# Kernel tuning notes

Hardware: AMD Instinct MI355X
Metric: run time of the kernel (lower is better)

Reference implementation:

```python
import jax, jax.numpy as jnp
import numpy as np

BATCH = 256
INPUT_DIM = 64
LEVELS = 100
HV_DIM = 10000


def setup_inputs() -> dict:
    key = jax.random.key(0)
    kx, kb = jax.random.split(key)
    x = jax.random.uniform(kx, (BATCH, INPUT_DIM), dtype=jnp.float32)
    base = jax.random.normal(kb, (INPUT_DIM, LEVELS, HV_DIM), dtype=jnp.float32)
    # buffer is L2-normalized along hv_dim at construction time
    base = base / jnp.linalg.norm(base, axis=-1, keepdims=True)
    return {"x": x, "base_hvs": base}


def reference(x, base_hvs):
    D, L, H = base_hvs.shape
    B = x.shape[0]
    xn = jnp.clip(x * (L - 1), 0.0, float(L - 1))          # [B, D]
    lo = jnp.floor(xn).astype(jnp.int32)                    # [B, D]
    hi = jnp.clip(lo + 1, 0, L - 1)                         # [B, D]
    alpha = xn - lo.astype(x.dtype)                         # [B, D]

    def step(acc, inputs):
        bhv, l, h, a = inputs    # bhv: [L, H], l/h/a: [B]
        hv_low = bhv[l]          # [B, H] gather
        hv_high = bhv[h]         # [B, H] gather
        a = a[:, None]
        return acc + (1.0 - a) * hv_low + a * hv_high, None

    init = jnp.zeros((B, H), dtype=x.dtype)
    encoded, _ = jax.lax.scan(step, init, (base_hvs, lo.T, hi.T, alpha.T))
    return encoded / jnp.linalg.norm(encoded, axis=-1, keepdims=True)
```

## Files before the change

### kernel.cpp

```cpp
#include <hip/hip_runtime.h>

#define BATCH   256
#define DIMS    64
#define LEVELS  100
#define HVD     10000

__global__ __launch_bounds__(256) void encode_kernel(
    const float* __restrict__ x,
    const float* __restrict__ base,
    float* __restrict__ out)
{
    __shared__ int   s_off_lo[256];
    __shared__ int   s_off_hi[256];
    __shared__ float s_alpha[256];

    const int tid    = threadIdx.x;
    const int b_tile = blockIdx.x;
    const int h0     = blockIdx.y * 256;

    {
        const int bl = tid >> 6;
        const int d  = tid & 63;
        const int b  = b_tile * 4 + bl;
        float xv = x[b * DIMS + d];
        float xn = xv * (float)(LEVELS - 1);
        xn = fminf(fmaxf(xn, 0.0f), (float)(LEVELS - 1));
        float fl = floorf(xn);
        int   lo = (int)fl;
        int   hi = lo + 1; if (hi > LEVELS - 1) hi = LEVELS - 1;
        s_off_lo[tid] = (d * LEVELS + lo) * HVD;
        s_off_hi[tid] = (d * LEVELS + hi) * HVD;
        s_alpha[tid]  = xn - fl;
    }
    __syncthreads();

    const int bl   = tid >> 6;
    const int lane = tid & 63;
    const int h    = h0 + lane * 4;
    if (h >= HVD) return;
    const int b    = b_tile * 4 + bl;

    const int ebase = bl * 64;
    float4 acc = make_float4(0.f, 0.f, 0.f, 0.f);

    #pragma unroll 8
    for (int d = 0; d < DIMS; ++d) {
        const int   off_lo = s_off_lo[ebase + d];
        const int   off_hi = s_off_hi[ebase + d];
        const float a      = s_alpha[ebase + d];
        const float wl     = 1.0f - a;
        float4 vlo = *(const float4*)(base + off_lo + h);
        float4 vhi = *(const float4*)(base + off_hi + h);
        acc.x += wl * vlo.x + a * vhi.x;
        acc.y += wl * vlo.y + a * vhi.y;
        acc.z += wl * vlo.z + a * vhi.z;
        acc.w += wl * vlo.w + a * vhi.w;
    }

    *(float4*)(out + b * HVD + h) = acc;
}

__global__ __launch_bounds__(256) void normalize_kernel(float* __restrict__ out)
{
    const int b   = blockIdx.x;
    const int tid = threadIdx.x;
    float* row = out + b * HVD;
    const float4* row4 = (const float4*)row;

    float ss = 0.f;
    for (int i = tid; i < HVD / 4; i += 256) {
        float4 v = row4[i];
        ss += v.x * v.x + v.y * v.y + v.z * v.z + v.w * v.w;
    }

    __shared__ float red[256];
    red[tid] = ss;
    __syncthreads();
    #pragma unroll
    for (int s = 128; s > 0; s >>= 1) {
        if (tid < s) red[tid] += red[tid + s];
        __syncthreads();
    }
    const float inv = rsqrtf(red[0]);

    for (int i = tid; i < HVD / 4; i += 256) {
        float4 v = ((float4*)row)[i];
        v.x *= inv; v.y *= inv; v.z *= inv; v.w *= inv;
        ((float4*)row)[i] = v;
    }
}

extern "C" void kernel_launch(void* const* d_in, const int* in_sizes, int n_in,
                              void* d_out, int out_size, void* d_ws, size_t ws_size,
                              hipStream_t stream)
{
    const float* x    = (const float*)d_in[0];
    const float* base = (const float*)d_in[1];
    float*       out  = (float*)d_out;

    dim3 grid(BATCH / 4, (HVD + 255) / 256);
    encode_kernel<<<grid, 256, 0, stream>>>(x, base, out);
    normalize_kernel<<<BATCH, 256, 0, stream>>>(out);
}
```

Measured before the change: 402.7 us.

## Stage base-vector chunks in LDS and split reduction over input dims

The encoder now tiles along the hypervector dimension. Each block loads all 100 levels of one input dim for a 64-wide column slice into shared memory, and all 256 batch rows gather from there, so each base element is read from global memory once rather than once per batch tile. The 64 input dims are split across 8 blocks that write partial sums to workspace. The finish kernel sums those partials, then normalizes. This cuts the redundant global gather traffic on the large base tensor, at the cost of a workspace round trip of 8x the output size and 16 float4 accumulators per thread.

```diff
diff --git a/kernel.cpp b/kernel.cpp
--- a/kernel.cpp
+++ b/kernel.cpp
@@ -4,73 +4,106 @@
 #define DIMS    64
 #define LEVELS  100
 #define HVD     10000
+#define WH      64
+#define NHT     157
+#define DSPLIT  8
+#define DPER    8
+#define LSTRIDE 68
 
 __global__ __launch_bounds__(256) void encode_kernel(
     const float* __restrict__ x,
     const float* __restrict__ base,
-    float* __restrict__ out)
+    float* __restrict__ partial)
 {
-    __shared__ int   s_off_lo[256];
-    __shared__ int   s_off_hi[256];
-    __shared__ float s_alpha[256];
+    __shared__ float s_chunk[LEVELS * LSTRIDE];
+    __shared__ int   s_lohi[DPER][BATCH];
+    __shared__ float s_a[DPER][BATCH];
 
-    const int tid    = threadIdx.x;
-    const int b_tile = blockIdx.x;
-    const int h0     = blockIdx.y * 256;
+    const int tid   = threadIdx.x;
+    const int htile = blockIdx.x;
+    const int split = blockIdx.y;
+    const int h0    = htile * WH;
+    const int d0    = split * DPER;
 
-    {
-        const int bl = tid >> 6;
-        const int d  = tid & 63;
-        const int b  = b_tile * 4 + bl;
-        float xv = x[b * DIMS + d];
-        float xn = xv * (float)(LEVELS - 1);
-        xn = fminf(fmaxf(xn, 0.0f), (float)(LEVELS - 1));
+    for (int k = 0; k < DPER; ++k) {
+        const int dl = k;
+        const int b  = tid;
+        float xv = x[b * DIMS + d0 + dl];
+        float xn = fminf(fmaxf(xv * (float)(LEVELS - 1), 0.0f), (float)(LEVELS - 1));
         float fl = floorf(xn);
         int   lo = (int)fl;
-        int   hi = lo + 1; if (hi > LEVELS - 1) hi = LEVELS - 1;
-        s_off_lo[tid] = (d * LEVELS + lo) * HVD;
-        s_off_hi[tid] = (d * LEVELS + hi) * HVD;
-        s_alpha[tid]  = xn - fl;
-    }
-    __syncthreads();
-
-    const int bl   = tid >> 6;
-    const int lane = tid & 63;
-    const int h    = h0 + lane * 4;
-    if (h >= HVD) return;
-    const int b    = b_tile * 4 + bl;
-
-    const int ebase = bl * 64;
-    float4 acc = make_float4(0.f, 0.f, 0.f, 0.f);
-
-    #pragma unroll 8
-    for (int d = 0; d < DIMS; ++d) {
-        const int   off_lo = s_off_lo[ebase + d];
-        const int   off_hi = s_off_hi[ebase + d];
-        const float a      = s_alpha[ebase + d];
-        const float wl     = 1.0f - a;
-        float4 vlo = *(const float4*)(base + off_lo + h);
-        float4 vhi = *(const float4*)(base + off_hi + h);
-        acc.x += wl * vlo.x + a * vhi.x;
-        acc.y += wl * vlo.y + a * vhi.y;
-        acc.z += wl * vlo.z + a * vhi.z;
-        acc.w += wl * vlo.w + a * vhi.w;
+        int   hi = lo < LEVELS - 1 ? lo + 1 : LEVELS - 1;
+        s_lohi[dl][b] = (lo * LSTRIDE) | ((hi * LSTRIDE) << 16);
+        s_a[dl][b]    = xn - fl;
     }
 
-    *(float4*)(out + b * HVD + h) = acc;
+    const int g  = tid >> 4;
+    const int ci = (tid & 15) * 4;
+    const int wvalid = (HVD - h0) < WH ? (HVD - h0) : WH;
+
+    float4 acc[16];
+    #pragma unroll
+    for (int j = 0; j < 16; ++j) acc[j] = make_float4(0.f, 0.f, 0.f, 0.f);
+
+    for (int dc = 0; dc < DPER; ++dc) {
+        __syncthreads();
+
+        const float* src = base + ((size_t)(d0 + dc) * LEVELS) * (size_t)HVD + h0;
+        for (int i = tid; i < LEVELS * (WH / 4); i += 256) {
+            const int l  = i >> 4;
+            const int cc = (i & 15) * 4;
+            if (cc < wvalid) {
+                float4 v = *(const float4*)(src + (size_t)l * HVD + cc);
+                *(float4*)(&s_chunk[l * LSTRIDE + cc]) = v;
+            }
+        }
+        __syncthreads();
+
+        #pragma unroll
+        for (int j = 0; j < 16; ++j) {
+            const int   b    = g * 16 + j;
+            const int   lohi = s_lohi[dc][b];
+            const float a    = s_a[dc][b];
+            const int   olo  = lohi & 0xffff;
+            const int   ohi  = lohi >> 16;
+            const float wl   = 1.0f - a;
+            float4 vlo = *(const float4*)(&s_chunk[olo + ci]);
+            float4 vhi = *(const float4*)(&s_chunk[ohi + ci]);
+            acc[j].x += wl * vlo.x + a * vhi.x;
+            acc[j].y += wl * vlo.y + a * vhi.y;
+            acc[j].z += wl * vlo.z + a * vhi.z;
+            acc[j].w += wl * vlo.w + a * vhi.w;
+        }
+    }
+
+    if (ci < wvalid) {
+        float* dst = partial + ((size_t)split * BATCH) * (size_t)HVD + h0 + ci;
+        #pragma unroll
+        for (int j = 0; j < 16; ++j) {
+            const int b = g * 16 + j;
+            *(float4*)(dst + (size_t)b * HVD) = acc[j];
+        }
+    }
 }
 
-__global__ __launch_bounds__(256) void normalize_kernel(float* __restrict__ out)
+__global__ __launch_bounds__(256) void finish_kernel(
+    const float* __restrict__ partial,
+    float* __restrict__ out)
 {
     const int b   = blockIdx.x;
     const int tid = threadIdx.x;
-    float* row = out + b * HVD;
-    const float4* row4 = (const float4*)row;
 
     float ss = 0.f;
     for (int i = tid; i < HVD / 4; i += 256) {
-        float4 v = row4[i];
-        ss += v.x * v.x + v.y * v.y + v.z * v.z + v.w * v.w;
+        float4 s = make_float4(0.f, 0.f, 0.f, 0.f);
+        #pragma unroll
+        for (int sp = 0; sp < DSPLIT; ++sp) {
+            const float4 v = *(const float4*)(partial +
+                ((size_t)sp * BATCH + b) * (size_t)HVD + i * 4);
+            s.x += v.x; s.y += v.y; s.z += v.z; s.w += v.w;
+        }
+        *(float4*)(out + (size_t)b * HVD + i * 4) = s;
+        ss += s.x * s.x + s.y * s.y + s.z * s.z + s.w * s.w;
     }
 
     __shared__ float red[256];
@@ -84,9 +117,9 @@
     const float inv = rsqrtf(red[0]);
 
     for (int i = tid; i < HVD / 4; i += 256) {
-        float4 v = ((float4*)row)[i];
+        float4 v = *(float4*)(out + (size_t)b * HVD + i * 4);
         v.x *= inv; v.y *= inv; v.z *= inv; v.w *= inv;
-        ((float4*)row)[i] = v;
+        *(float4*)(out + (size_t)b * HVD + i * 4) = v;
     }
 }
 
@@ -97,8 +130,9 @@
     const float* x    = (const float*)d_in[0];
     const float* base = (const float*)d_in[1];
     float*       out  = (float*)d_out;
+    float*       part = (float*)d_ws;
 
-    dim3 grid(BATCH / 4, (HVD + 255) / 256);
-    encode_kernel<<<grid, 256, 0, stream>>>(x, base, out);
-    normalize_kernel<<<BATCH, 256, 0, stream>>>(out);
+    dim3 grid(NHT, DSPLIT);
+    encode_kernel<<<grid, 256, 0, stream>>>(x, base, part);
+    finish_kernel<<<BATCH, 256, 0, stream>>>(part, out);
 }
```

Result: slower. 428.2 us (+6.3%).
